# Kernel optimization log

Hardware: AMD Instinct MI355X
Metric: run time of the kernel (lower is better)

Reference implementation:

```python
import jax, jax.numpy as jnp
import numpy as np

B, T, D, H = 1024, 200, 128, 128


def setup_inputs() -> dict:
    key = jax.random.key(0)
    k1, k2, k3, k4 = jax.random.split(key, 4)
    item_his_eb = jax.random.normal(k1, (B, T, D), dtype=jnp.float32)
    seq_len = jax.random.randint(k2, (B,), 0, T, dtype=jnp.int32)
    # TF GRUCell packs [r, u] gates in one matmul over concat([x, h]).
    W_gate = jax.random.normal(k3, (D + H, 2 * H), dtype=jnp.float32) * (1.0 / np.sqrt(D + H))
    b_gate = jnp.ones((2 * H,), dtype=jnp.float32)  # TF GRUCell bias init = 1.0
    W_cand = jax.random.normal(k4, (D + H, H), dtype=jnp.float32) * (1.0 / np.sqrt(D + H))
    b_cand = jnp.zeros((H,), dtype=jnp.float32)
    return {"item_his_eb": item_his_eb, "seq_len": seq_len,
            "W_gate": W_gate, "b_gate": b_gate,
            "W_cand": W_cand, "b_cand": b_cand}


def reference(item_his_eb, seq_len, W_gate, b_gate, W_cand, b_cand):
    # dynamic_rnn(GRUCell(H)) with sequence_length masking.
    # Outputs are zero and state is held for steps t >= seq_len.
    Bq, Tq, Dq = item_his_eb.shape
    Hq = W_cand.shape[1]
    x_tbd = jnp.transpose(item_his_eb, (1, 0, 2))  # [T, B, D]

    def step(h, inp):
        x_t, t = inp  # x_t: [B, D], t: scalar int
        gates = jax.nn.sigmoid(jnp.concatenate([x_t, h], axis=-1) @ W_gate + b_gate)
        r, u = jnp.split(gates, 2, axis=-1)  # each [B, H]
        c = jnp.tanh(jnp.concatenate([x_t, r * h], axis=-1) @ W_cand + b_cand)
        h_new = u * h + (1.0 - u) * c
        valid = (t < seq_len)[:, None]  # [B, 1]
        h_next = jnp.where(valid, h_new, h)
        y = jnp.where(valid, h_new, jnp.zeros_like(h_new))
        return h_next, y

    h0 = jnp.zeros((Bq, Hq), dtype=item_his_eb.dtype)
    _, ys = jax.lax.scan(step, h0, (x_tbd, jnp.arange(Tq)))
    return jnp.transpose(ys, (1, 0, 2))  # [B, T, H]
```

## Files before the change

### kernel.cpp

```cpp
#include <hip/hip_runtime.h>

#define T_SZ 200
#define H_SZ 128

typedef __attribute__((ext_vector_type(8))) short    bf16x8;
typedef __attribute__((ext_vector_type(4))) float    f32x4;
typedef __attribute__((ext_vector_type(4))) int      i32x4;
typedef __attribute__((ext_vector_type(2))) unsigned u32x2;

__device__ __forceinline__ unsigned short f2bf(float f) {
  unsigned u = __builtin_bit_cast(unsigned, f);
  u += 0x7fffu + ((u >> 16) & 1u);
  return (unsigned short)(u >> 16);
}
__device__ __forceinline__ unsigned cvt_pk_bf16(float a, float b) {
  unsigned r;
  asm("v_cvt_pk_bf16_f32 %0, %1, %2" : "=v"(r) : "v"(a), "v"(b));
  return r;
}
__device__ __forceinline__ float sigmoid_fast(float x) {
  float e = __builtin_amdgcn_exp2f(-1.442695041f * x);
  return __builtin_amdgcn_rcpf(1.0f + e);
}
__device__ __forceinline__ float tanh_fast(float x) {
  float e = __builtin_amdgcn_exp2f(2.885390082f * x);
  return 1.0f - 2.0f * __builtin_amdgcn_rcpf(e + 1.0f);
}
__device__ __forceinline__ void ldsbar() {
  __asm__ __volatile__("" ::: "memory");
  __builtin_amdgcn_s_waitcnt(0xc07f);
  __builtin_amdgcn_s_barrier();
  __asm__ __volatile__("" ::: "memory");
}

__global__ __launch_bounds__(512, 1) void gru_fused(
    const float* __restrict__ X,
    const int*   __restrict__ seq_len,
    const float* __restrict__ Wg,
    const float* __restrict__ bg,
    const float* __restrict__ Wc,
    const float* __restrict__ bc,
    float* __restrict__ Y)
{
  __shared__ unsigned short hA[16 * 136];
  __shared__ unsigned short rhA[16 * 136];
  __shared__ unsigned short xA[2][16 * 136];
  __shared__ float hT[128 * 20];
  __shared__ float ubuf[128 * 20];

  const int tid  = threadIdx.x;
  const int lane = tid & 63;
  const int w    = tid >> 6;
  const int m16  = lane & 15;
  const int q    = lane >> 4;

  bf16x8 wgf[2][8];
  float  gbias[2];
  #pragma unroll
  for (int nt = 0; nt < 2; ++nt) {
    int col = w * 32 + nt * 16 + m16;
    gbias[nt] = bg[col];
    #pragma unroll
    for (int kb = 0; kb < 8; ++kb) {
      bf16x8 f;
      #pragma unroll
      for (int j = 0; j < 8; ++j)
        f[j] = (short)f2bf(Wg[(size_t)(kb * 32 + q * 8 + j) * 256 + col]);
      wgf[nt][kb] = f;
    }
  }
  const int colc = w * 16 + m16;
  bf16x8 wcf[8];
  float  cbias = bc[colc];
  #pragma unroll
  for (int kb = 0; kb < 8; ++kb) {
    bf16x8 f;
    #pragma unroll
    for (int j = 0; j < 8; ++j)
      f[j] = (short)f2bf(Wc[(size_t)(kb * 32 + q * 8 + j) * 128 + colc]);
    wcf[kb] = f;
  }

  const int bt = blockIdx.x;
  int slen[4];
  #pragma unroll
  for (int i = 0; i < 4; ++i) slen[i] = seq_len[bt * 16 + q * 4 + i];

  float h[4] = {0.f, 0.f, 0.f, 0.f};

  for (int idx = tid; idx < 16 * 136; idx += 512) hA[idx] = 0;
  for (int idx = tid; idx < 128 * 20; idx += 512) hT[idx] = 0.f;

  const int xrow = tid >> 5;
  const int xk4  = (tid & 31) * 4;
  const float* xbase = X + (size_t)(bt * 16 + xrow) * T_SZ * 128 + xk4;

  auto xload = [&](int t, f32x4& r) {
    r = *(const f32x4*)(xbase + (size_t)t * 128);
  };
  auto xstage = [&](int buf, const f32x4& r) {
    unsigned d0 = cvt_pk_bf16(r.x, r.y);
    unsigned d1 = cvt_pk_bf16(r.z, r.w);
    *(u32x2*)&xA[buf][xrow * 136 + xk4] = (u32x2){d0, d1};
  };

  f32x4 x0r, x1r, xrE, xrO;
  xload(0, x0r); xload(1, x1r);
  xstage(0, x0r); xstage(1, x1r);
  xload(2, xrE); xload(3, xrO);
  ldsbar();

  f32x4 axA[2], axB[2], ccA, ccB;
  {
    bf16x8 xaf[4];
    #pragma unroll
    for (int kb = 0; kb < 4; ++kb)
      xaf[kb] = __builtin_bit_cast(bf16x8, *(const i32x4*)&xA[0][m16 * 136 + kb * 32 + q * 8]);
    f32x4 cc = { cbias, cbias, cbias, cbias };
    #pragma unroll
    for (int kb = 0; kb < 4; ++kb)
      cc = __builtin_amdgcn_mfma_f32_16x16x32_bf16(xaf[kb], wcf[kb], cc, 0, 0, 0);
    ccA = cc;
    #pragma unroll
    for (int nt = 0; nt < 2; ++nt) {
      f32x4 a = { gbias[nt], gbias[nt], gbias[nt], gbias[nt] };
      #pragma unroll
      for (int kb = 0; kb < 4; ++kb)
        a = __builtin_amdgcn_mfma_f32_16x16x32_bf16(xaf[kb], wgf[nt][kb], a, 0, 0, 0);
      axA[nt] = a;
    }
  }
  ldsbar();

  float* const ybase = Y + (size_t)(bt * 16 + q * 4) * T_SZ * H_SZ + colc;

  auto step = [&](int t, f32x4& xreg, f32x4* axin, f32x4& ccin,
                  f32x4* axout, f32x4& ccout) {
    bf16x8 haf[4];
    #pragma unroll
    for (int kb = 0; kb < 4; ++kb)
      haf[kb] = __builtin_bit_cast(bf16x8, *(const i32x4*)&hA[m16 * 136 + kb * 32 + q * 8]);
    f32x4 hv0, hv1;
    if (w < 4) {
      hv0 = *(const f32x4*)&hT[(w * 32 + m16) * 20 + q * 4];
      hv1 = *(const f32x4*)&hT[(w * 32 + 16 + m16) * 20 + q * 4];
    }
    if (t < 198) xstage(t & 1, xreg);
    if (t < 196) xload(t + 4, xreg);

    float racc[2][4];
    #pragma unroll
    for (int nt = 0; nt < 2; ++nt) {
      f32x4 a = { 0.f, 0.f, 0.f, 0.f }, b = { 0.f, 0.f, 0.f, 0.f };
      a = __builtin_amdgcn_mfma_f32_16x16x32_bf16(haf[0], wgf[nt][4], a, 0, 0, 0);
      a = __builtin_amdgcn_mfma_f32_16x16x32_bf16(haf[1], wgf[nt][5], a, 0, 0, 0);
      b = __builtin_amdgcn_mfma_f32_16x16x32_bf16(haf[2], wgf[nt][6], b, 0, 0, 0);
      b = __builtin_amdgcn_mfma_f32_16x16x32_bf16(haf[3], wgf[nt][7], b, 0, 0, 0);
      #pragma unroll
      for (int i = 0; i < 4; ++i)
        racc[nt][i] = sigmoid_fast(axin[nt][i] + a[i] + b[i]);
    }

    if (w < 4) {
      #pragma unroll
      for (int nt = 0; nt < 2; ++nt) {
        const f32x4 hv = nt ? hv1 : hv0;
        unsigned p01 = cvt_pk_bf16(racc[nt][0] * hv.x, racc[nt][1] * hv.y);
        unsigned p23 = cvt_pk_bf16(racc[nt][2] * hv.z, racc[nt][3] * hv.w);
        int col = w * 32 + nt * 16 + m16;
        rhA[(q * 4 + 0) * 136 + col] = (unsigned short)(p01 & 0xffffu);
        rhA[(q * 4 + 1) * 136 + col] = (unsigned short)(p01 >> 16);
        rhA[(q * 4 + 2) * 136 + col] = (unsigned short)(p23 & 0xffffu);
        rhA[(q * 4 + 3) * 136 + col] = (unsigned short)(p23 >> 16);
      }
    } else {
      #pragma unroll
      for (int nt = 0; nt < 2; ++nt) {
        int colu = (w - 4) * 32 + nt * 16 + m16;
        f32x4 v = { racc[nt][0], racc[nt][1], racc[nt][2], racc[nt][3] };
        *(f32x4*)&ubuf[colu * 20 + q * 4] = v;
      }
    }
    ldsbar();

    bf16x8 xaf2[4];
    if (t < 199) {
      const unsigned short* xb = xA[(t + 1) & 1];
      #pragma unroll
      for (int kb = 0; kb < 4; ++kb)
        xaf2[kb] = __builtin_bit_cast(bf16x8, *(const i32x4*)&xb[m16 * 136 + kb * 32 + q * 8]);
    }
    bf16x8 rhf[4];
    #pragma unroll
    for (int kb = 0; kb < 4; ++kb)
      rhf[kb] = __builtin_bit_cast(bf16x8, *(const i32x4*)&rhA[m16 * 136 + kb * 32 + q * 8]);
    f32x4 uv = *(const f32x4*)&ubuf[colc * 20 + q * 4];

    if (t < 199) {
      f32x4 cc = { cbias, cbias, cbias, cbias };
      #pragma unroll
      for (int kb = 0; kb < 4; ++kb)
        cc = __builtin_amdgcn_mfma_f32_16x16x32_bf16(xaf2[kb], wcf[kb], cc, 0, 0, 0);
      ccout = cc;
      #pragma unroll
      for (int nt = 0; nt < 2; ++nt) {
        f32x4 a = { gbias[nt], gbias[nt], gbias[nt], gbias[nt] };
        #pragma unroll
        for (int kb = 0; kb < 4; ++kb)
          a = __builtin_amdgcn_mfma_f32_16x16x32_bf16(xaf2[kb], wgf[nt][kb], a, 0, 0, 0);
        axout[nt] = a;
      }
    }

    f32x4 ca = { 0.f, 0.f, 0.f, 0.f }, cb = { 0.f, 0.f, 0.f, 0.f };
    ca = __builtin_amdgcn_mfma_f32_16x16x32_bf16(rhf[0], wcf[4], ca, 0, 0, 0);
    ca = __builtin_amdgcn_mfma_f32_16x16x32_bf16(rhf[1], wcf[5], ca, 0, 0, 0);
    cb = __builtin_amdgcn_mfma_f32_16x16x32_bf16(rhf[2], wcf[6], cb, 0, 0, 0);
    cb = __builtin_amdgcn_mfma_f32_16x16x32_bf16(rhf[3], wcf[7], cb, 0, 0, 0);

    #pragma unroll
    for (int i = 0; i < 4; ++i) {
      float c  = tanh_fast(ccin[i] + ca[i] + cb[i]);
      float hn = uv[i] * (h[i] - c) + c;
      bool valid = (t < slen[i]);
      float hvz = valid ? hn : h[i];
      h[i] = hvz;
      ybase[(size_t)i * T_SZ * H_SZ + (size_t)t * H_SZ] = valid ? hn : 0.0f;
    }
    unsigned hp01 = cvt_pk_bf16(h[0], h[1]);
    unsigned hp23 = cvt_pk_bf16(h[2], h[3]);
    hA[(q * 4 + 0) * 136 + colc] = (unsigned short)(hp01 & 0xffffu);
    hA[(q * 4 + 1) * 136 + colc] = (unsigned short)(hp01 >> 16);
    hA[(q * 4 + 2) * 136 + colc] = (unsigned short)(hp23 & 0xffffu);
    hA[(q * 4 + 3) * 136 + colc] = (unsigned short)(hp23 >> 16);
    *(f32x4*)&hT[colc * 20 + q * 4] = (f32x4){ h[0], h[1], h[2], h[3] };
    ldsbar();
  };

  for (int t = 0; t < 200; t += 2) {
    step(t,     xrE, axA, ccA, axB, ccB);
    step(t + 1, xrO, axB, ccB, axA, ccA);
  }
}

extern "C" void kernel_launch(void* const* d_in, const int* in_sizes, int n_in,
                              void* d_out, int out_size, void* d_ws, size_t ws_size,
                              hipStream_t stream) {
  const float* X   = (const float*)d_in[0];
  const int*   seq = (const int*)  d_in[1];
  const float* Wg  = (const float*)d_in[2];
  const float* bg  = (const float*)d_in[3];
  const float* Wc  = (const float*)d_in[4];
  const float* bc  = (const float*)d_in[5];
  float* Y = (float*)d_out;
  (void)d_ws; (void)ws_size;

  hipLaunchKernelGGL(gru_fused, dim3(64), dim3(512), 0, stream,
                     X, seq, Wg, bg, Wc, bc, Y);
}
```

Before: 361.0 us.

## Align gate columns with candidate columns to keep r and u in registers

Each wave's gate columns are remapped so the r and u columns it computes match the hidden columns it owns for the candidate step. r*h can then use the register-held h, and u stays in registers. This removes the fp32 hT and ubuf shared buffers, their per-step stores and loads, and the split where warps 0-3 and 4-7 took different branches. In exchange the u sigmoid is delayed, and the candidate recurrent MFMAs are moved ahead of the x-projection MFMAs, which may change how latency is hidden.

```diff
diff --git a/kernel.cpp b/kernel.cpp
--- a/kernel.cpp
+++ b/kernel.cpp
@@ -45,8 +45,6 @@
   __shared__ unsigned short hA[16 * 136];
   __shared__ unsigned short rhA[16 * 136];
   __shared__ unsigned short xA[2][16 * 136];
-  __shared__ float hT[128 * 20];
-  __shared__ float ubuf[128 * 20];
 
   const int tid  = threadIdx.x;
   const int lane = tid & 63;
@@ -58,7 +56,7 @@
   float  gbias[2];
   #pragma unroll
   for (int nt = 0; nt < 2; ++nt) {
-    int col = w * 32 + nt * 16 + m16;
+    int col = nt * 128 + w * 16 + m16;
     gbias[nt] = bg[col];
     #pragma unroll
     for (int kb = 0; kb < 8; ++kb) {
@@ -89,7 +87,6 @@
   float h[4] = {0.f, 0.f, 0.f, 0.f};
 
   for (int idx = tid; idx < 16 * 136; idx += 512) hA[idx] = 0;
-  for (int idx = tid; idx < 128 * 20; idx += 512) hT[idx] = 0.f;
 
   const int xrow = tid >> 5;
   const int xk4  = (tid & 31) * 4;
@@ -140,49 +137,40 @@
     #pragma unroll
     for (int kb = 0; kb < 4; ++kb)
       haf[kb] = __builtin_bit_cast(bf16x8, *(const i32x4*)&hA[m16 * 136 + kb * 32 + q * 8]);
-    f32x4 hv0, hv1;
-    if (w < 4) {
-      hv0 = *(const f32x4*)&hT[(w * 32 + m16) * 20 + q * 4];
-      hv1 = *(const f32x4*)&hT[(w * 32 + 16 + m16) * 20 + q * 4];
-    }
+
     if (t < 198) xstage(t & 1, xreg);
     if (t < 196) xload(t + 4, xreg);
 
-    float racc[2][4];
-    #pragma unroll
-    for (int nt = 0; nt < 2; ++nt) {
-      f32x4 a = { 0.f, 0.f, 0.f, 0.f }, b = { 0.f, 0.f, 0.f, 0.f };
-      a = __builtin_amdgcn_mfma_f32_16x16x32_bf16(haf[0], wgf[nt][4], a, 0, 0, 0);
-      a = __builtin_amdgcn_mfma_f32_16x16x32_bf16(haf[1], wgf[nt][5], a, 0, 0, 0);
-      b = __builtin_amdgcn_mfma_f32_16x16x32_bf16(haf[2], wgf[nt][6], b, 0, 0, 0);
-      b = __builtin_amdgcn_mfma_f32_16x16x32_bf16(haf[3], wgf[nt][7], b, 0, 0, 0);
-      #pragma unroll
-      for (int i = 0; i < 4; ++i)
-        racc[nt][i] = sigmoid_fast(axin[nt][i] + a[i] + b[i]);
-    }
-
-    if (w < 4) {
-      #pragma unroll
-      for (int nt = 0; nt < 2; ++nt) {
-        const f32x4 hv = nt ? hv1 : hv0;
-        unsigned p01 = cvt_pk_bf16(racc[nt][0] * hv.x, racc[nt][1] * hv.y);
-        unsigned p23 = cvt_pk_bf16(racc[nt][2] * hv.z, racc[nt][3] * hv.w);
-        int col = w * 32 + nt * 16 + m16;
-        rhA[(q * 4 + 0) * 136 + col] = (unsigned short)(p01 & 0xffffu);
-        rhA[(q * 4 + 1) * 136 + col] = (unsigned short)(p01 >> 16);
-        rhA[(q * 4 + 2) * 136 + col] = (unsigned short)(p23 & 0xffffu);
-        rhA[(q * 4 + 3) * 136 + col] = (unsigned short)(p23 >> 16);
-      }
-    } else {
-      #pragma unroll
-      for (int nt = 0; nt < 2; ++nt) {
-        int colu = (w - 4) * 32 + nt * 16 + m16;
-        f32x4 v = { racc[nt][0], racc[nt][1], racc[nt][2], racc[nt][3] };
-        *(f32x4*)&ubuf[colu * 20 + q * 4] = v;
-      }
-    }
+    f32x4 ra = { 0.f, 0.f, 0.f, 0.f }, rb = { 0.f, 0.f, 0.f, 0.f };
+    ra = __builtin_amdgcn_mfma_f32_16x16x32_bf16(haf[0], wgf[0][4], ra, 0, 0, 0);
+    ra = __builtin_amdgcn_mfma_f32_16x16x32_bf16(haf[1], wgf[0][5], ra, 0, 0, 0);
+    rb = __builtin_amdgcn_mfma_f32_16x16x32_bf16(haf[2], wgf[0][6], rb, 0, 0, 0);
+    rb = __builtin_amdgcn_mfma_f32_16x16x32_bf16(haf[3], wgf[0][7], rb, 0, 0, 0);
+    f32x4 ua = { 0.f, 0.f, 0.f, 0.f }, ub = { 0.f, 0.f, 0.f, 0.f };
+    ua = __builtin_amdgcn_mfma_f32_16x16x32_bf16(haf[0], wgf[1][4], ua, 0, 0, 0);
+    ua = __builtin_amdgcn_mfma_f32_16x16x32_bf16(haf[1], wgf[1][5], ua, 0, 0, 0);
+    ub = __builtin_amdgcn_mfma_f32_16x16x32_bf16(haf[2], wgf[1][6], ub, 0, 0, 0);
+    ub = __builtin_amdgcn_mfma_f32_16x16x32_bf16(haf[3], wgf[1][7], ub, 0, 0, 0);
+    f32x4 uacc;
+    #pragma unroll
+    for (int i = 0; i < 4; ++i) uacc[i] = axin[1][i] + ua[i] + ub[i];
+
+    float rh0 = sigmoid_fast(axin[0][0] + ra[0] + rb[0]) * h[0];
+    float rh1 = sigmoid_fast(axin[0][1] + ra[1] + rb[1]) * h[1];
+    float rh2 = sigmoid_fast(axin[0][2] + ra[2] + rb[2]) * h[2];
+    float rh3 = sigmoid_fast(axin[0][3] + ra[3] + rb[3]) * h[3];
+    unsigned rp01 = cvt_pk_bf16(rh0, rh1);
+    unsigned rp23 = cvt_pk_bf16(rh2, rh3);
+    rhA[(q * 4 + 0) * 136 + colc] = (unsigned short)(rp01 & 0xffffu);
+    rhA[(q * 4 + 1) * 136 + colc] = (unsigned short)(rp01 >> 16);
+    rhA[(q * 4 + 2) * 136 + colc] = (unsigned short)(rp23 & 0xffffu);
+    rhA[(q * 4 + 3) * 136 + colc] = (unsigned short)(rp23 >> 16);
     ldsbar();
 
+    bf16x8 rhf[4];
+    #pragma unroll
+    for (int kb = 0; kb < 4; ++kb)
+      rhf[kb] = __builtin_bit_cast(bf16x8, *(const i32x4*)&rhA[m16 * 136 + kb * 32 + q * 8]);
     bf16x8 xaf2[4];
     if (t < 199) {
       const unsigned short* xb = xA[(t + 1) & 1];
@@ -190,11 +178,12 @@
       for (int kb = 0; kb < 4; ++kb)
         xaf2[kb] = __builtin_bit_cast(bf16x8, *(const i32x4*)&xb[m16 * 136 + kb * 32 + q * 8]);
     }
-    bf16x8 rhf[4];
-    #pragma unroll
-    for (int kb = 0; kb < 4; ++kb)
-      rhf[kb] = __builtin_bit_cast(bf16x8, *(const i32x4*)&rhA[m16 * 136 + kb * 32 + q * 8]);
-    f32x4 uv = *(const f32x4*)&ubuf[colc * 20 + q * 4];
+
+    f32x4 ca = { 0.f, 0.f, 0.f, 0.f }, cb = { 0.f, 0.f, 0.f, 0.f };
+    ca = __builtin_amdgcn_mfma_f32_16x16x32_bf16(rhf[0], wcf[4], ca, 0, 0, 0);
+    ca = __builtin_amdgcn_mfma_f32_16x16x32_bf16(rhf[1], wcf[5], ca, 0, 0, 0);
+    cb = __builtin_amdgcn_mfma_f32_16x16x32_bf16(rhf[2], wcf[6], cb, 0, 0, 0);
+    cb = __builtin_amdgcn_mfma_f32_16x16x32_bf16(rhf[3], wcf[7], cb, 0, 0, 0);
 
     if (t < 199) {
       f32x4 cc = { cbias, cbias, cbias, cbias };
@@ -212,11 +201,9 @@
       }
     }
 
-    f32x4 ca = { 0.f, 0.f, 0.f, 0.f }, cb = { 0.f, 0.f, 0.f, 0.f };
-    ca = __builtin_amdgcn_mfma_f32_16x16x32_bf16(rhf[0], wcf[4], ca, 0, 0, 0);
-    ca = __builtin_amdgcn_mfma_f32_16x16x32_bf16(rhf[1], wcf[5], ca, 0, 0, 0);
-    cb = __builtin_amdgcn_mfma_f32_16x16x32_bf16(rhf[2], wcf[6], cb, 0, 0, 0);
-    cb = __builtin_amdgcn_mfma_f32_16x16x32_bf16(rhf[3], wcf[7], cb, 0, 0, 0);
+    f32x4 uv;
+    #pragma unroll
+    for (int i = 0; i < 4; ++i) uv[i] = sigmoid_fast(uacc[i]);
 
     #pragma unroll
     for (int i = 0; i < 4; ++i) {
@@ -233,7 +220,6 @@
     hA[(q * 4 + 1) * 136 + colc] = (unsigned short)(hp01 >> 16);
     hA[(q * 4 + 2) * 136 + colc] = (unsigned short)(hp23 & 0xffffu);
     hA[(q * 4 + 3) * 136 + colc] = (unsigned short)(hp23 >> 16);
-    *(f32x4*)&hT[colc * 20 + q * 4] = (f32x4){ h[0], h[1], h[2], h[3] };
     ldsbar();
   };
 
```

New measurement: 346.6 us. -4.0%, faster.
